# Kernel optimization log

Hardware: AMD Instinct MI355X
Metric: run time of the kernel (lower is better)

Reference implementation:

```python
import jax, jax.numpy as jnp
import numpy as np

B = 4096
OBS_DIM = 1024
E_OUT = 512
H1 = 2048
H2 = 2048


def setup_inputs() -> dict:
    key = jax.random.key(0)
    ks = jax.random.split(key, 12)
    def kaiming(k, shape, fan_in):
        return jax.random.normal(k, shape, dtype=jnp.float32) * np.float32(np.sqrt(2.0 / fan_in))
    obs = jax.random.normal(ks[0], (B, OBS_DIM), dtype=jnp.float32)
    # lineare: Linear(obs_dim, e_outputs), torch weight shape [out, in]
    We = kaiming(ks[1], (E_OUT, OBS_DIM), OBS_DIM)
    be = jax.random.normal(ks[2], (E_OUT,), dtype=jnp.float32) * 0.01
    # obs_dim attention heads, each Linear(e_outputs, 2), stacked
    attn_W = kaiming(ks[3], (OBS_DIM, E_OUT, 2), E_OUT)
    attn_b = jax.random.normal(ks[4], (OBS_DIM, 2), dtype=jnp.float32) * 0.01
    # v_net: Linear(obs_dim,H1)+tanh, Linear(H1,H2)+[dropout(eval:no-op)]+tanh, Linear(H2,1)
    W1 = kaiming(ks[5], (H1, OBS_DIM), OBS_DIM)
    b1 = jnp.zeros((H1,), dtype=jnp.float32)
    W2 = kaiming(ks[6], (H2, H1), H1)
    b2 = jnp.zeros((H2,), dtype=jnp.float32)
    W3 = kaiming(ks[7], (1, H2), H2)
    b3 = jnp.zeros((1,), dtype=jnp.float32)
    return {"obs": obs, "We": We, "be": be, "attn_W": attn_W, "attn_b": attn_b,
            "W1": W1, "b1": b1, "W2": W2, "b2": b2, "W3": W3, "b3": b3}


def reference(obs, We, be, attn_W, attn_b, W1, b1, W2, b2, W3, b3):
    # e = tanh(lineare(obs)) : [B, E_OUT]
    e = jnp.tanh(obs @ We.T + be)
    # all obs_dim attention heads batched into one contraction: [B, OBS_DIM, 2]
    logits = jnp.einsum('be,oec->boc', e, attn_W) + attn_b
    # softmax over the 2 logits, keep prob of class 1 -> Attention [B, OBS_DIM]
    attention = jax.nn.softmax(logits, axis=-1)[..., 1]
    state_attention = obs * attention
    # v_net (eval mode: dropout is identity)
    h = jnp.tanh(state_attention @ W1.T + b1)
    h = jnp.tanh(h @ W2.T + b2)
    v = jnp.squeeze(h @ W3.T + b3, -1)  # [B]
    return (v, attention)
```

## Files before the change

kernel.cpp:

```cpp
#include <hip/hip_runtime.h>
#include <hip/hip_bf16.h>

typedef unsigned short u16;
typedef u16 u16x4 __attribute__((ext_vector_type(4)));
typedef u16 u16x8 __attribute__((ext_vector_type(8)));
typedef __bf16 bf16x8 __attribute__((ext_vector_type(8)));
typedef float f32x4 __attribute__((ext_vector_type(4)));

__device__ __forceinline__ u16 f2bf(float f) {
  unsigned u = __float_as_uint(f);
  u += 0x7FFFu + ((u >> 16) & 1u);
  return (u16)(u >> 16);
}
__device__ __forceinline__ float bf2f(u16 h) {
  return __uint_as_float(((unsigned)h) << 16);
}
__device__ __forceinline__ float tanh_fast(float x) {
  float t = __expf(2.0f * x);
  return 1.0f - 2.0f / (t + 1.0f);
}
__device__ __forceinline__ float sigmoid_fast(float x) {
  return 1.0f / (1.0f + __expf(-x));
}

__device__ __forceinline__ void glds16(const u16* g, u16* l) {
  __builtin_amdgcn_global_load_lds(
      (const __attribute__((address_space(1))) unsigned int*)g,
      (__attribute__((address_space(3))) unsigned int*)l, 16, 0, 0);
}

__device__ __forceinline__ void cvt4(const float* __restrict__ s, u16* __restrict__ d, int q) {
  float4 v = ((const float4*)s)[q];
  u16x4 o = { f2bf(v.x), f2bf(v.y), f2bf(v.z), f2bf(v.w) };
  ((u16x4*)d)[q] = o;
}

__global__ __launch_bounds__(256)
void prep_kernel(const float* __restrict__ obs, const float* __restrict__ We,
                 const float* __restrict__ W1, const float* __restrict__ W2,
                 const float* __restrict__ aW, const float* __restrict__ ab,
                 u16* __restrict__ obs_b, u16* __restrict__ We_b,
                 u16* __restrict__ W1_b, u16* __restrict__ W2_b,
                 u16* __restrict__ Wd, float* __restrict__ bd,
                 float* __restrict__ vzero) {
  int q = blockIdx.x * 256 + threadIdx.x;
  if (q < 1024) ((float4*)vzero)[q] = (float4){0.f, 0.f, 0.f, 0.f};
  if (q < 1048576) { cvt4(obs, obs_b, q); return; }
  q -= 1048576;
  if (q < 131072) { cvt4(We, We_b, q); return; }
  q -= 131072;
  if (q < 524288) { cvt4(W1, W1_b, q); return; }
  q -= 524288;
  if (q < 1048576) { cvt4(W2, W2_b, q); return; }
  q -= 1048576;
  if (q < 131072) {
    int i0 = q * 4;
    int o = i0 >> 9, e0 = i0 & 511;
    const float* p = aW + (size_t)o * 1024 + e0 * 2;
    float4 v0 = *(const float4*)p;
    float4 v1 = *(const float4*)(p + 4);
    u16x4 od = { f2bf(v0.y - v0.x), f2bf(v0.w - v0.z),
                 f2bf(v1.y - v1.x), f2bf(v1.w - v1.z) };
    *(u16x4*)(Wd + i0) = od;
    if (q < 256) {
      float4 a0 = *(const float4*)(ab + q * 8);
      float4 a1 = *(const float4*)(ab + q * 8 + 4);
      float4 ob = { a0.y - a0.x, a0.w - a0.z, a1.y - a1.x, a1.w - a1.z };
      *(float4*)(bd + q * 4) = ob;
    }
  }
}

template <int BM, int BN, int EP>
__global__ __launch_bounds__(256, 4)
void gemm_bt(const u16* __restrict__ A, const u16* __restrict__ Bt,
             int N, int K,
             const float* __restrict__ bias,
             u16* __restrict__ outb, float* __restrict__ outf,
             const u16* __restrict__ obsb, u16* __restrict__ sa,
             const float* __restrict__ W3, const float* __restrict__ b3,
             float* __restrict__ vout) {
  constexpr int CA = BM / 32;
  constexpr int CB = BN / 32;
  constexpr int MI = BM / 32;
  constexpr int NJ = BN / 32;

  __shared__ __align__(16) u16 As[BM * 64];
  __shared__ __align__(16) u16 Bs[BN * 64];

  const int tid = threadIdx.x;
  const int lane = tid & 63;
  const int wave = tid >> 6;
  const int bm = blockIdx.x, bn = blockIdx.y;

  const int r0 = tid >> 3;
  const int kc = (tid & 7) * 8;

  const u16* gA = A + (size_t)(bm * BM + r0) * K + kc;
  const u16* gB = Bt + (size_t)(bn * BN + r0) * K + kc;
  u16* lA = As + r0 * 64 + kc;
  u16* lB = Bs + r0 * 64 + kc;

  const int wm = (wave >> 1) * (BM / 2);
  const int wn = (wave & 1) * (BN / 2);
  const int fr = lane & 15;
  const int koff = (lane >> 4) * 8;

  f32x4 acc[MI][NJ];
#pragma unroll
  for (int i = 0; i < MI; ++i)
#pragma unroll
    for (int j = 0; j < NJ; ++j)
      acc[i][j] = (f32x4){0.f, 0.f, 0.f, 0.f};

  const int T = K >> 6;
  for (int k = 0; k < T; ++k) {
    if (k) __syncthreads();
#pragma unroll
    for (int q = 0; q < CA; ++q)
      glds16(gA + (size_t)q * 32 * K, lA + q * 32 * 64);
#pragma unroll
    for (int q = 0; q < CB; ++q)
      glds16(gB + (size_t)q * 32 * K, lB + q * 32 * 64);
    gA += 64; gB += 64;
    __syncthreads();

#pragma unroll
    for (int s = 0; s < 2; ++s) {
      bf16x8 a[MI], b[NJ];
#pragma unroll
      for (int i = 0; i < MI; ++i)
        a[i] = *(const bf16x8*)(As + (wm + i * 16 + fr) * 64 + s * 32 + koff);
#pragma unroll
      for (int j = 0; j < NJ; ++j)
        b[j] = *(const bf16x8*)(Bs + (wn + j * 16 + fr) * 64 + s * 32 + koff);
#pragma unroll
      for (int i = 0; i < MI; ++i)
#pragma unroll
        for (int j = 0; j < NJ; ++j)
          acc[i][j] = __builtin_amdgcn_mfma_f32_16x16x32_bf16(a[i], b[j], acc[i][j], 0, 0, 0);
    }
  }

  if constexpr (EP == 2) {
    float vpart[MI][4];
#pragma unroll
    for (int i = 0; i < MI; ++i)
#pragma unroll
      for (int r = 0; r < 4; ++r) vpart[i][r] = 0.f;
#pragma unroll
    for (int j = 0; j < NJ; ++j) {
      const int col = bn * BN + wn + j * 16 + fr;
      const float bv = bias[col];
      const float w3 = W3[col];
#pragma unroll
      for (int i = 0; i < MI; ++i)
#pragma unroll
        for (int r = 0; r < 4; ++r)
          vpart[i][r] += tanh_fast(acc[i][j][r] + bv) * w3;
    }
    const bool lead = (fr == 0);
    const bool addb = (bn == 0) && ((wave & 1) == 0);
#pragma unroll
    for (int i = 0; i < MI; ++i)
#pragma unroll
      for (int r = 0; r < 4; ++r) {
        float p = vpart[i][r];
        p += __shfl_xor(p, 8);
        p += __shfl_xor(p, 4);
        p += __shfl_xor(p, 2);
        p += __shfl_xor(p, 1);
        if (lead) {
          const int row = bm * BM + wm + i * 16 + (lane >> 4) * 4 + r;
          atomicAdd(vout + row, addb ? p + b3[0] : p);
        }
      }
  } else {
#pragma unroll
    for (int j = 0; j < NJ; ++j) {
      const int col = bn * BN + wn + j * 16 + fr;
      const float bv = bias[col];
#pragma unroll
      for (int i = 0; i < MI; ++i) {
#pragma unroll
        for (int r = 0; r < 4; ++r) {
          const int row = bm * BM + wm + i * 16 + (lane >> 4) * 4 + r;
          const float x = acc[i][j][r] + bv;
          const size_t idx = (size_t)row * N + col;
          if constexpr (EP == 0) {
            outb[idx] = f2bf(tanh_fast(x));
          } else {
            const float att = sigmoid_fast(x);
            outf[idx] = att;
            sa[idx] = f2bf(bf2f(obsb[idx]) * att);
          }
        }
      }
    }
  }
}

extern "C" void kernel_launch(void* const* d_in, const int* in_sizes, int n_in,
                              void* d_out, int out_size, void* d_ws, size_t ws_size,
                              hipStream_t stream) {
  const float* obs   = (const float*)d_in[0];
  const float* We    = (const float*)d_in[1];
  const float* be    = (const float*)d_in[2];
  const float* attnW = (const float*)d_in[3];
  const float* attnb = (const float*)d_in[4];
  const float* W1    = (const float*)d_in[5];
  const float* b1    = (const float*)d_in[6];
  const float* W2    = (const float*)d_in[7];
  const float* b2    = (const float*)d_in[8];
  const float* W3    = (const float*)d_in[9];
  const float* b3    = (const float*)d_in[10];
  float* out = (float*)d_out;

  char* ws = (char*)d_ws;
  u16*   We_b  = (u16*)(ws + 0x00000000);
  u16*   Wd_b  = (u16*)(ws + 0x00100000);
  u16*   W1_b  = (u16*)(ws + 0x00200000);
  u16*   W2_b  = (u16*)(ws + 0x00600000);
  float* bd    = (float*)(ws + 0x00E00000);
  u16*   obs_b = (u16*)(ws + 0x00E01000);
  u16*   e_b   = (u16*)(ws + 0x01601000);
  u16*   sa_b  = (u16*)(ws + 0x01A01000);
  u16*   h1_b  = (u16*)(ws + 0x02201000);

  prep_kernel<<<11264, 256, 0, stream>>>(obs, We, W1, W2, attnW, attnb,
                                         obs_b, We_b, W1_b, W2_b, Wd_b, bd, out);

  gemm_bt<64, 64, 0><<<dim3(64, 8), 256, 0, stream>>>(
      obs_b, We_b, 512, 1024, be, e_b, nullptr, nullptr, nullptr, nullptr, nullptr, nullptr);
  gemm_bt<128, 64, 1><<<dim3(32, 16), 256, 0, stream>>>(
      e_b, Wd_b, 1024, 512, bd, nullptr, out + 4096, obs_b, sa_b, nullptr, nullptr, nullptr);
  gemm_bt<128, 128, 0><<<dim3(32, 16), 256, 0, stream>>>(
      sa_b, W1_b, 2048, 1024, b1, h1_b, nullptr, nullptr, nullptr, nullptr, nullptr, nullptr);
  gemm_bt<128, 128, 2><<<dim3(32, 16), 256, 0, stream>>>(
      h1_b, W2_b, 2048, 2048, b2, nullptr, nullptr, nullptr, nullptr, W3, b3, out);
}
```

Baseline: 222.9 us.

## Double-buffer GEMM LDS tiles and XOR-swizzle LDS layout

The GEMM main loop now uses two LDS buffers, so the global-to-LDS loads for the next K tile are issued while MFMAs run on the current tile. This removes one barrier per iteration and hides load latency. The LDS layout is XOR-swizzled on the 16-byte chunk index to reduce bank conflicts on the fragment reads. Launch bounds drop to 2 blocks per SM, so occupancy falls in exchange for twice the LDS per block. The loop assumes an even tile count, which holds for K=512, 1024 and 2048.

```diff
diff --git a/kernel.cpp b/kernel.cpp
--- a/kernel.cpp
+++ b/kernel.cpp
@@ -72,7 +72,7 @@
 }
 
 template <int BM, int BN, int EP>
-__global__ __launch_bounds__(256, 4)
+__global__ __launch_bounds__(256, 2)
 void gemm_bt(const u16* __restrict__ A, const u16* __restrict__ Bt,
              int N, int K,
              const float* __restrict__ bias,
@@ -85,8 +85,10 @@
   constexpr int MI = BM / 32;
   constexpr int NJ = BN / 32;
 
-  __shared__ __align__(16) u16 As[BM * 64];
-  __shared__ __align__(16) u16 Bs[BN * 64];
+  __shared__ __align__(16) u16 As0[BM * 64];
+  __shared__ __align__(16) u16 Bs0[BN * 64];
+  __shared__ __align__(16) u16 As1[BM * 64];
+  __shared__ __align__(16) u16 Bs1[BN * 64];
 
   const int tid = threadIdx.x;
   const int lane = tid & 63;
@@ -94,17 +96,16 @@
   const int bm = blockIdx.x, bn = blockIdx.y;
 
   const int r0 = tid >> 3;
-  const int kc = (tid & 7) * 8;
-
-  const u16* gA = A + (size_t)(bm * BM + r0) * K + kc;
-  const u16* gB = Bt + (size_t)(bn * BN + r0) * K + kc;
-  u16* lA = As + r0 * 64 + kc;
-  u16* lB = Bs + r0 * 64 + kc;
+  const int kcs = ((tid & 7) ^ (r0 & 7)) * 8;
+
+  const u16* gA = A + (size_t)(bm * BM + r0) * K + kcs;
+  const u16* gB = Bt + (size_t)(bn * BN + r0) * K + kcs;
 
   const int wm = (wave >> 1) * (BM / 2);
   const int wn = (wave & 1) * (BN / 2);
   const int fr = lane & 15;
-  const int koff = (lane >> 4) * 8;
+  const int hi = lane >> 4;
+  const int frx = fr & 7;
 
   f32x4 acc[MI][NJ];
 #pragma unroll
@@ -113,33 +114,45 @@
     for (int j = 0; j < NJ; ++j)
       acc[i][j] = (f32x4){0.f, 0.f, 0.f, 0.f};
 
-  const int T = K >> 6;
-  for (int k = 0; k < T; ++k) {
-    if (k) __syncthreads();
+  auto stage = [&](u16* __restrict__ dA, u16* __restrict__ dB) {
 #pragma unroll
     for (int q = 0; q < CA; ++q)
-      glds16(gA + (size_t)q * 32 * K, lA + q * 32 * 64);
+      glds16(gA + (size_t)q * 32 * K, dA + tid * 8 + q * 2048);
 #pragma unroll
     for (int q = 0; q < CB; ++q)
-      glds16(gB + (size_t)q * 32 * K, lB + q * 32 * 64);
+      glds16(gB + (size_t)q * 32 * K, dB + tid * 8 + q * 2048);
     gA += 64; gB += 64;
-    __syncthreads();
-
+  };
+
+  auto compute = [&](const u16* sA, const u16* sB) {
 #pragma unroll
     for (int s = 0; s < 2; ++s) {
+      const int ck = ((s * 4 + hi) ^ frx) * 8;
       bf16x8 a[MI], b[NJ];
 #pragma unroll
       for (int i = 0; i < MI; ++i)
-        a[i] = *(const bf16x8*)(As + (wm + i * 16 + fr) * 64 + s * 32 + koff);
+        a[i] = *(const bf16x8*)(sA + (wm + i * 16 + fr) * 64 + ck);
 #pragma unroll
       for (int j = 0; j < NJ; ++j)
-        b[j] = *(const bf16x8*)(Bs + (wn + j * 16 + fr) * 64 + s * 32 + koff);
+        b[j] = *(const bf16x8*)(sB + (wn + j * 16 + fr) * 64 + ck);
 #pragma unroll
       for (int i = 0; i < MI; ++i)
 #pragma unroll
         for (int j = 0; j < NJ; ++j)
           acc[i][j] = __builtin_amdgcn_mfma_f32_16x16x32_bf16(a[i], b[j], acc[i][j], 0, 0, 0);
     }
+  };
+
+  const int T = K >> 6;
+  stage(As0, Bs0);
+  __syncthreads();
+  for (int k = 0; k < T; k += 2) {
+    stage(As1, Bs1);
+    compute(As0, Bs0);
+    __syncthreads();
+    if (k + 2 < T) stage(As0, Bs0);
+    compute(As1, Bs1);
+    __syncthreads();
   }
 
   if constexpr (EP == 2) {
```

Result: faster. 189.9 us (-14.8%).
